# Kernel optimization log

Measured on AMD Instinct MI355X. Metric: run time of the kernel, lower is better.

## Reference

```python
import jax, jax.numpy as jnp
import numpy as np

B, T, D = 2, 2048, 1024
E, K, FF = 8, 2, 4096


def setup_inputs() -> dict:
    key = jax.random.key(0)
    ks = jax.random.split(key, 4)
    scale = 0.02
    return {
        "x": jax.random.normal(ks[0], (B, T, D), jnp.float32),
        "gate_w": jax.random.normal(ks[1], (D, E), jnp.float32) * scale,
        "gate_b": jnp.zeros((E,), jnp.float32),
        "w1": jax.random.normal(ks[2], (E, D, FF), jnp.float32) * scale,
        "b1": jnp.zeros((E, FF), jnp.float32),
        "w2": jax.random.normal(ks[3], (E, FF, D), jnp.float32) * scale,
        "b2": jnp.zeros((E, D), jnp.float32),
    }


def reference(x, gate_w, gate_b, w1, b1, w2, b2):
    # x: (B,T,D). Original runs every expert densely over all tokens then masks;
    # since mask*x == x at selected positions and output is re-masked, the math
    # equals: output[t] = sum_k softmax(topk_vals)[k] * expert_{idx_k}(x)[t].
    n_experts = w1.shape[0]
    gate_logits = x @ gate_w + gate_b                      # (B,T,E)
    topk_vals, topk_idx = jax.lax.top_k(gate_logits, K)    # (B,T,K)
    topk_w = jax.nn.softmax(topk_vals, axis=-1)            # (B,T,K)
    onehot = jax.nn.one_hot(topk_idx, n_experts, dtype=x.dtype)  # (B,T,K,E)
    comb = jnp.sum(onehot * topk_w[..., None], axis=2)     # (B,T,E) combine weights

    # Dense per-expert FFN over all tokens (faithful to original redundant compute)
    h = jax.nn.gelu(jnp.einsum('btd,edf->ebtf', x, w1) + b1[:, None, None, :],
                    approximate=False)                      # (E,B,T,FF)
    y = jnp.einsum('ebtf,efd->ebtd', h, w2) + b2[:, None, None, :]  # (E,B,T,D)
    output = jnp.einsum('ebtd,bte->btd', y, comb)           # (B,T,D)

    expert_counts = jnp.sum(onehot, axis=(0, 1, 2)).astype(jnp.float32)  # (E,)
    return output, gate_logits, topk_idx, expert_counts
```

## Files before the change

kernel.cpp:

```cpp
#include <hip/hip_runtime.h>
#include <math.h>

#define NTOK 4096
#define DIM  1024
#define NE   8
#define FF   4096

#define OUT_LOGITS 4194304
#define OUT_IDX    4227072
#define OUT_CNT    4235264

typedef unsigned short u16;
typedef __bf16 bf16x8 __attribute__((ext_vector_type(8)));
typedef float  f32x4  __attribute__((ext_vector_type(4)));
typedef u16    u16x8  __attribute__((ext_vector_type(8)));

__device__ __forceinline__ u16 f2bf(float f) {
  union { float f; unsigned u; } v; v.f = f;
  unsigned r = v.u + 0x7fffu + ((v.u >> 16) & 1u);
  return (u16)(r >> 16);
}

__device__ __forceinline__ float gelu_f(float v) {
  float u = v * (0.7978845608f + 0.0356774081f * v * v);
  float e = __expf(2.f * u);
  float t = 1.f - 2.f / (e + 1.f);
  return 0.5f * v * (1.f + t);
}

__device__ __forceinline__ void gload_lds16(const u16* g, u16* l) {
  __builtin_amdgcn_global_load_lds(
      (const __attribute__((address_space(1))) void*)(g),
      (__attribute__((address_space(3))) void*)(l), 16, 0, 0);
}

__global__ __launch_bounds__(256) void transpose_cvt2_kernel(
    const float* __restrict__ w1, u16* __restrict__ w1t,
    const float* __restrict__ w2, u16* __restrict__ w2t) {
  __shared__ float tile[4096];
  int id = blockIdx.x;
  const float* in; u16* out; int R, C, xt, yt, z;
  if (id < 8192) {
    in = w1; out = w1t; R = DIM; C = FF;
    xt = id & 63; yt = (id >> 6) & 15; z = id >> 10;
  } else {
    int i2 = id - 8192;
    in = w2; out = w2t; R = FF; C = DIM;
    xt = i2 & 15; yt = (i2 >> 4) & 63; z = i2 >> 10;
  }
  in  += (size_t)z * R * C;
  out += (size_t)z * R * C;
  const int c0 = xt * 64, r0 = yt * 64;
  const int t = threadIdx.x;

  {
    int cc = t & 15, rr = t >> 4;
    #pragma unroll
    for (int p = 0; p < 4; p++) {
      int r = rr + p * 16;
      float4 v = *(const float4*)(in + (size_t)(r0 + r) * C + c0 + cc * 4);
      *(float4*)&tile[r * 64 + ((cc ^ (r >> 3)) << 2)] = v;
    }
  }
  __syncthreads();
  {
    int h = t & 7, cg = t >> 3;
    #pragma unroll
    for (int p = 0; p < 2; p++) {
      int c = p * 32 + cg;
      int base = ((((c >> 2) ^ h) << 2)) + (c & 3);
      u16x8 o;
      #pragma unroll
      for (int j = 0; j < 8; j++)
        o[j] = f2bf(tile[(h * 8 + j) * 64 + base]);
      *(u16x8*)(out + (size_t)(c0 + c) * R + r0 + h * 8) = o;
    }
  }
}

__global__ __launch_bounds__(256) void gate_kernel(const float* __restrict__ x,
                                                   const float* __restrict__ gw,
                                                   const float* __restrict__ gb,
                                                   float* __restrict__ out,
                                                   int2* __restrict__ tk_idx,
                                                   float2* __restrict__ tk_w) {
  int wave = threadIdx.x >> 6, lane = threadIdx.x & 63;
  int token = blockIdx.x * 4 + wave;
  const float* xr = x + (size_t)token * DIM + lane * 16;
  float acc[NE];
  #pragma unroll
  for (int e = 0; e < NE; e++) acc[e] = 0.f;
  #pragma unroll
  for (int c = 0; c < 16; c += 4) {
    float4 xv = *(const float4*)(xr + c);
    const float* gwr = gw + (size_t)(lane * 16 + c) * NE;
    float xs[4] = {xv.x, xv.y, xv.z, xv.w};
    #pragma unroll
    for (int q = 0; q < 4; q++)
      #pragma unroll
      for (int e = 0; e < NE; e++)
        acc[e] += xs[q] * gwr[q * NE + e];
  }
  #pragma unroll
  for (int off = 32; off; off >>= 1)
    #pragma unroll
    for (int e = 0; e < NE; e++)
      acc[e] += __shfl_down(acc[e], off);

  if (lane == 0) {
    float lg[NE];
    #pragma unroll
    for (int e = 0; e < NE; e++) {
      lg[e] = acc[e] + gb[e];
      out[OUT_LOGITS + token * NE + e] = lg[e];
    }
    int i0 = 0; float v0 = lg[0];
    #pragma unroll
    for (int e = 1; e < NE; e++) if (lg[e] > v0) { v0 = lg[e]; i0 = e; }
    int i1 = -1; float v1 = -1e30f;
    #pragma unroll
    for (int e = 0; e < NE; e++) if (e != i0 && lg[e] > v1) { v1 = lg[e]; i1 = e; }
    float ex = expf(v1 - v0);
    float s = 1.f + ex;
    out[OUT_IDX + token * 2]     = (float)i0;
    out[OUT_IDX + token * 2 + 1] = (float)i1;
    tk_idx[token] = make_int2(i0, i1);
    tk_w[token]   = make_float2(1.f / s, ex / s);
  }
}

__global__ __launch_bounds__(512) void build_lists_kernel(
    const int2* __restrict__ tk_idx, const float2* __restrict__ tk_w,
    int* __restrict__ counts, int* __restrict__ offsets,
    int* __restrict__ tok_list, float* __restrict__ wt_list,
    float* __restrict__ cnt_out) {
  __shared__ int s_cnt[NE];
  int e = threadIdx.x >> 6, lane = threadIdx.x & 63;
  int cnt = 0;
  for (int base = 0; base < NTOK; base += 64) {
    int2 idx = tk_idx[base + lane];
    cnt += __popcll(__ballot(idx.x == e || idx.y == e));
  }
  if (lane == 0) s_cnt[e] = cnt;
  __syncthreads();
  int off = 0;
  for (int ee = 0; ee < e; ee++) off += s_cnt[ee];
  if (lane == 0) {
    counts[e]  = s_cnt[e];
    offsets[e] = off;
    cnt_out[e] = (float)s_cnt[e];
  }
  int pos = off;
  for (int base = 0; base < NTOK; base += 64) {
    int tok = base + lane;
    int2 idx = tk_idx[tok];
    float2 w = tk_w[tok];
    bool m0 = (idx.x == e), m1 = (idx.y == e);
    bool m = m0 || m1;
    unsigned long long mask = __ballot(m);
    if (m) {
      int p = pos + __popcll(mask & ((1ull << lane) - 1ull));
      tok_list[p] = tok;
      wt_list[p]  = m0 ? w.x : w.y;
    }
    pos += __popcll(mask);
  }
}

__global__ __launch_bounds__(256) void gather_x_kernel(const float* __restrict__ x,
                                                       const int* __restrict__ tok_list,
                                                       u16* __restrict__ xg) {
  int g = blockIdx.x;
  int tok = tok_list[g];
  int c = threadIdx.x * 4;
  float4 v = *(const float4*)(x + (size_t)tok * DIM + c);
  ushort4 o;
  o.x = f2bf(v.x); o.y = f2bf(v.y); o.z = f2bf(v.z); o.w = f2bf(v.w);
  *(ushort4*)(xg + (size_t)g * DIM + c) = o;
}

template <int MODE, int BM, int BN>
__global__ __launch_bounds__(512, 2) void moe_gemm2_kernel(
    const u16* __restrict__ Abase, const u16* __restrict__ Bbase,
    const float* __restrict__ bias,
    const int* __restrict__ counts, const int* __restrict__ offsets,
    const int* __restrict__ tok_list, const float* __restrict__ wt_list,
    u16* __restrict__ Hout, float* __restrict__ Out) {
  constexpr int KT = (MODE == 0) ? DIM : FF;
  constexpr int NT = (MODE == 0) ? FF : DIM;
  constexpr int LA = BM / 64;
  constexpr int LB = BN / 64;
  constexpr int MR = BM / 32;
  constexpr int NR = BN / 64;
  constexpr int ASZ = BM * 64;
  constexpr int BSZ = BN * 64;
  constexpr int NTILES = (MODE == 0) ? (KT / 64) : (KT / 128);

  extern __shared__ u16 sm[];

  const int zz = blockIdx.z;
  const int e  = (MODE == 1) ? (zz >> 1) : zz;
  const int koff = (MODE == 1) ? ((zz & 1) * (KT / 2)) : 0;
  const int ne = counts[e];
  const int m0 = blockIdx.y * BM;
  if (m0 >= ne) return;
  const int n0   = blockIdx.x * BN;
  const int offs = offsets[e];

  const int t = threadIdx.x;
  const int wave = t >> 6, lane = t & 63;
  const int quad = lane >> 4, l16 = lane & 15;
  const int wmb = (wave & 1) * (BM / 2);
  const int wnb = (wave >> 1) * (BN / 4);

  const u16* aptr[LA];
  const u16* bptr[LB];
  #pragma unroll
  for (int p = 0; p < LA; p++) {
    int idx = p * 512 + t;
    int row = idx >> 3, c = idx & 7;
    int clog = c ^ (row & 7);
    int s = m0 + row; if (s > ne - 1) s = ne - 1;
    aptr[p] = Abase + (size_t)(offs + s) * KT + koff + clog * 8;
  }
  #pragma unroll
  for (int p = 0; p < LB; p++) {
    int idx = p * 512 + t;
    int row = idx >> 3, c = idx & 7;
    int clog = c ^ (row & 7);
    bptr[p] = Bbase + ((size_t)e * NT + n0 + row) * KT + koff + clog * 8;
  }

  auto stage = [&](int buf, int k0) {
    #pragma unroll
    for (int p = 0; p < LA; p++)
      gload_lds16(aptr[p] + k0, sm + buf * ASZ + (p * 512 + t) * 8);
    #pragma unroll
    for (int p = 0; p < LB; p++)
      gload_lds16(bptr[p] + k0, sm + 2 * ASZ + buf * BSZ + (p * 512 + t) * 8);
  };

  const int xrow = l16 & 7;
  const int xo[2] = { ((0 + quad) ^ xrow) * 8, ((4 + quad) ^ xrow) * 8 };
  const int abase0 = (wmb + l16) * 64;
  const int bbase0 = 2 * ASZ + (wnb + l16) * 64;

  f32x4 acc[MR][NR];
  #pragma unroll
  for (int i = 0; i < MR; i++)
    #pragma unroll
    for (int j = 0; j < NR; j++)
      acc[i][j] = (f32x4){0.f, 0.f, 0.f, 0.f};

  stage(0, 0);
  __syncthreads();
  int cur = 0;
  for (int kt = 0; kt < NTILES; ++kt) {
    if (kt + 1 < NTILES) stage(cur ^ 1, (kt + 1) * 64);
    const u16* As = sm + cur * ASZ;
    const u16* Bs = sm + cur * BSZ;
    #pragma unroll
    for (int kk = 0; kk < 2; kk++) {
      bf16x8 a[MR], b[NR];
      #pragma unroll
      for (int i = 0; i < MR; i++) a[i] = *(const bf16x8*)&As[abase0 + i * 1024 + xo[kk]];
      #pragma unroll
      for (int j = 0; j < NR; j++) b[j] = *(const bf16x8*)&Bs[bbase0 + j * 1024 + xo[kk]];
      #pragma unroll
      for (int i = 0; i < MR; i++)
        #pragma unroll
        for (int j = 0; j < NR; j++)
          acc[i][j] = __builtin_amdgcn_mfma_f32_16x16x32_bf16(a[i], b[j], acc[i][j], 0, 0, 0);
    }
    __syncthreads();
    cur ^= 1;
  }

  if (MODE == 0) {
    const float* bb = bias + (size_t)e * FF + n0 + wnb;
    float bc[NR];
    #pragma unroll
    for (int j = 0; j < NR; j++) bc[j] = bb[j * 16 + l16];
    #pragma unroll
    for (int i = 0; i < MR; i++) {
      #pragma unroll
      for (int r = 0; r < 4; r++) {
        int s = m0 + wmb + i * 16 + quad * 4 + r;
        if (s < ne) {
          u16* hr = Hout + (size_t)(offs + s) * FF + n0 + wnb;
          #pragma unroll
          for (int j = 0; j < NR; j++)
            hr[j * 16 + l16] = f2bf(gelu_f(acc[i][j][r] + bc[j]));
        }
      }
    }
  } else {
    const float* bb = bias + (size_t)e * DIM + n0 + wnb;
    float bc[NR];
    #pragma unroll
    for (int j = 0; j < NR; j++) bc[j] = (zz & 1) ? 0.f : bb[j * 16 + l16];
    #pragma unroll
    for (int i = 0; i < MR; i++) {
      #pragma unroll
      for (int r = 0; r < 4; r++) {
        int s = m0 + wmb + i * 16 + quad * 4 + r;
        if (s < ne) {
          int   tok = tok_list[offs + s];
          float w   = wt_list[offs + s];
          float* orow = Out + (size_t)tok * DIM + n0 + wnb;
          #pragma unroll
          for (int j = 0; j < NR; j++)
            atomicAdd(&orow[j * 16 + l16], (acc[i][j][r] + bc[j]) * w);
        }
      }
    }
  }
}

extern "C" void kernel_launch(void* const* d_in, const int* in_sizes, int n_in,
                              void* d_out, int out_size, void* d_ws, size_t ws_size,
                              hipStream_t stream) {
  const float* x   = (const float*)d_in[0];
  const float* gw  = (const float*)d_in[1];
  const float* gb  = (const float*)d_in[2];
  const float* w1  = (const float*)d_in[3];
  const float* b1  = (const float*)d_in[4];
  const float* w2  = (const float*)d_in[5];
  const float* b2  = (const float*)d_in[6];
  float* out = (float*)d_out;
  char*  ws  = (char*)d_ws;

  u16* w1t = (u16*)(ws);
  u16* w2t = (u16*)(ws + 1ull * 67108864);
  u16* h   = (u16*)(ws + 2ull * 67108864);
  u16* xg  = (u16*)(ws + 3ull * 67108864);
  char* meta = ws + 3ull * 67108864 + 16777216;
  int*    counts   = (int*)(meta);
  int*    offsets  = (int*)(meta + 64);
  int*    tok_list = (int*)(meta + 128);
  float*  wt_list  = (float*)(meta + 128 + 32768);
  int2*   tk_idx   = (int2*)(meta + 128 + 2 * 32768);
  float2* tk_w     = (float2*)(meta + 128 + 2 * 32768 + 32768);
  (void)in_sizes; (void)n_in; (void)out_size; (void)ws_size;

  static bool attr_set = false;
  if (!attr_set) {
    hipFuncSetAttribute(reinterpret_cast<const void*>(moe_gemm2_kernel<0, 256, 256>),
                        hipFuncAttributeMaxDynamicSharedMemorySize, 131072);
    hipFuncSetAttribute(reinterpret_cast<const void*>(moe_gemm2_kernel<1, 128, 256>),
                        hipFuncAttributeMaxDynamicSharedMemorySize, 98304);
    attr_set = true;
  }

  hipMemsetAsync(out, 0, (size_t)OUT_LOGITS * 4, stream);

  transpose_cvt2_kernel<<<16384, 256, 0, stream>>>(w1, w1t, w2, w2t);
  gate_kernel<<<NTOK / 4, 256, 0, stream>>>(x, gw, gb, out, tk_idx, tk_w);
  build_lists_kernel<<<1, 512, 0, stream>>>(tk_idx, tk_w, counts, offsets, tok_list, wt_list,
                                            out + OUT_CNT);
  gather_x_kernel<<<2 * NTOK, 256, 0, stream>>>(x, tok_list, xg);

  moe_gemm2_kernel<0, 256, 256><<<dim3(FF / 256, NTOK / 256, NE), 512, 131072, stream>>>(
      xg, w1t, b1, counts, offsets, tok_list, wt_list, h, nullptr);
  moe_gemm2_kernel<1, 128, 256><<<dim3(DIM / 256, NTOK / 128, NE * 2), 512, 98304, stream>>>(
      h, w2t, b2, counts, offsets, tok_list, wt_list, nullptr, out);
}
```

Baseline: 636.3 us.

## Deepen MoE GEMM pipeline to four-stage ring with manual waitcnt and drop split-K

```diff
diff --git a/kernel.cpp b/kernel.cpp
--- a/kernel.cpp
+++ b/kernel.cpp
@@ -32,6 +32,17 @@
   __builtin_amdgcn_global_load_lds(
       (const __attribute__((address_space(1))) void*)(g),
       (__attribute__((address_space(3))) void*)(l), 16, 0, 0);
+}
+
+template <int N>
+__device__ __forceinline__ void wait_vm() {
+  if constexpr (N == 0)      asm volatile("s_waitcnt vmcnt(0)" ::: "memory");
+  else if constexpr (N == 1) asm volatile("s_waitcnt vmcnt(1)" ::: "memory");
+  else if constexpr (N == 2) asm volatile("s_waitcnt vmcnt(2)" ::: "memory");
+  else if constexpr (N == 3) asm volatile("s_waitcnt vmcnt(3)" ::: "memory");
+  else if constexpr (N == 4) asm volatile("s_waitcnt vmcnt(4)" ::: "memory");
+  else if constexpr (N == 6) asm volatile("s_waitcnt vmcnt(6)" ::: "memory");
+  else if constexpr (N == 8) asm volatile("s_waitcnt vmcnt(8)" ::: "memory");
 }
 
 __global__ __launch_bounds__(256) void transpose_cvt2_kernel(
@@ -180,7 +191,7 @@
 }
 
 template <int MODE, int BM, int BN>
-__global__ __launch_bounds__(512, 2) void moe_gemm2_kernel(
+__global__ __launch_bounds__(512, 2) void moe_gemm3_kernel(
     const u16* __restrict__ Abase, const u16* __restrict__ Bbase,
     const float* __restrict__ bias,
     const int* __restrict__ counts, const int* __restrict__ offsets,
@@ -188,19 +199,18 @@
     u16* __restrict__ Hout, float* __restrict__ Out) {
   constexpr int KT = (MODE == 0) ? DIM : FF;
   constexpr int NT = (MODE == 0) ? FF : DIM;
-  constexpr int LA = BM / 64;
-  constexpr int LB = BN / 64;
+  constexpr int NK = KT / 32;
+  constexpr int LA = BM / 128;
+  constexpr int LB = BN / 128;
+  constexpr int L  = LA + LB;
   constexpr int MR = BM / 32;
   constexpr int NR = BN / 64;
-  constexpr int ASZ = BM * 64;
-  constexpr int BSZ = BN * 64;
-  constexpr int NTILES = (MODE == 0) ? (KT / 64) : (KT / 128);
+  constexpr int ASLOT = BM * 32;
+  constexpr int BSLOT = BN * 32;
 
   extern __shared__ u16 sm[];
 
-  const int zz = blockIdx.z;
-  const int e  = (MODE == 1) ? (zz >> 1) : zz;
-  const int koff = (MODE == 1) ? ((zz & 1) * (KT / 2)) : 0;
+  const int e  = blockIdx.z;
   const int ne = counts[e];
   const int m0 = blockIdx.y * BM;
   if (m0 >= ne) return;
@@ -218,32 +228,31 @@
   #pragma unroll
   for (int p = 0; p < LA; p++) {
     int idx = p * 512 + t;
-    int row = idx >> 3, c = idx & 7;
-    int clog = c ^ (row & 7);
+    int row = idx >> 2, c = idx & 3;
+    int clog = c ^ ((row ^ (row >> 2)) & 3);
     int s = m0 + row; if (s > ne - 1) s = ne - 1;
-    aptr[p] = Abase + (size_t)(offs + s) * KT + koff + clog * 8;
+    aptr[p] = Abase + (size_t)(offs + s) * KT + clog * 8;
   }
   #pragma unroll
   for (int p = 0; p < LB; p++) {
     int idx = p * 512 + t;
-    int row = idx >> 3, c = idx & 7;
-    int clog = c ^ (row & 7);
-    bptr[p] = Bbase + ((size_t)e * NT + n0 + row) * KT + koff + clog * 8;
-  }
-
-  auto stage = [&](int buf, int k0) {
+    int row = idx >> 2, c = idx & 3;
+    int clog = c ^ ((row ^ (row >> 2)) & 3);
+    bptr[p] = Bbase + ((size_t)e * NT + n0 + row) * KT + clog * 8;
+  }
+
+  auto stage = [&](int slot, int kt) {
     #pragma unroll
     for (int p = 0; p < LA; p++)
-      gload_lds16(aptr[p] + k0, sm + buf * ASZ + (p * 512 + t) * 8);
+      gload_lds16(aptr[p] + kt * 32, sm + slot * ASLOT + (p * 512 + t) * 8);
     #pragma unroll
     for (int p = 0; p < LB; p++)
-      gload_lds16(bptr[p] + k0, sm + 2 * ASZ + buf * BSZ + (p * 512 + t) * 8);
+      gload_lds16(bptr[p] + kt * 32, sm + 4 * ASLOT + slot * BSLOT + (p * 512 + t) * 8);
   };
 
-  const int xrow = l16 & 7;
-  const int xo[2] = { ((0 + quad) ^ xrow) * 8, ((4 + quad) ^ xrow) * 8 };
-  const int abase0 = (wmb + l16) * 64;
-  const int bbase0 = 2 * ASZ + (wnb + l16) * 64;
+  const int csw = ((l16 ^ (l16 >> 2)) ^ quad) & 3;
+  const int aoff = (wmb + l16) * 32 + csw * 8;
+  const int boff = 4 * ASLOT + (wnb + l16) * 32 + csw * 8;
 
   f32x4 acc[MR][NR];
   #pragma unroll
@@ -252,29 +261,44 @@
     for (int j = 0; j < NR; j++)
       acc[i][j] = (f32x4){0.f, 0.f, 0.f, 0.f};
 
-  stage(0, 0);
-  __syncthreads();
-  int cur = 0;
-  for (int kt = 0; kt < NTILES; ++kt) {
-    if (kt + 1 < NTILES) stage(cur ^ 1, (kt + 1) * 64);
-    const u16* As = sm + cur * ASZ;
-    const u16* Bs = sm + cur * BSZ;
-    #pragma unroll
-    for (int kk = 0; kk < 2; kk++) {
-      bf16x8 a[MR], b[NR];
-      #pragma unroll
-      for (int i = 0; i < MR; i++) a[i] = *(const bf16x8*)&As[abase0 + i * 1024 + xo[kk]];
-      #pragma unroll
-      for (int j = 0; j < NR; j++) b[j] = *(const bf16x8*)&Bs[bbase0 + j * 1024 + xo[kk]];
-      #pragma unroll
-      for (int i = 0; i < MR; i++)
-        #pragma unroll
-        for (int j = 0; j < NR; j++)
-          acc[i][j] = __builtin_amdgcn_mfma_f32_16x16x32_bf16(a[i], b[j], acc[i][j], 0, 0, 0);
-    }
-    __syncthreads();
-    cur ^= 1;
-  }
+  auto compute = [&](int slot) {
+    const u16* As = sm + slot * ASLOT + aoff;
+    const u16* Bs = sm + slot * BSLOT + boff;
+    bf16x8 a[MR], b[NR];
+    #pragma unroll
+    for (int i = 0; i < MR; i++) a[i] = *(const bf16x8*)&As[i * 512];
+    #pragma unroll
+    for (int j = 0; j < NR; j++) b[j] = *(const bf16x8*)&Bs[j * 512];
+    __builtin_amdgcn_s_setprio(1);
+    #pragma unroll
+    for (int i = 0; i < MR; i++)
+      #pragma unroll
+      for (int j = 0; j < NR; j++)
+        acc[i][j] = __builtin_amdgcn_mfma_f32_16x16x32_bf16(a[i], b[j], acc[i][j], 0, 0, 0);
+    __builtin_amdgcn_s_setprio(0);
+  };
+
+  stage(0, 0); stage(1, 1); stage(2, 2);
+  wait_vm<2 * L>();
+  __builtin_amdgcn_s_barrier();
+  __builtin_amdgcn_sched_barrier(0);
+
+  for (int kt = 0; kt < NK - 3; ++kt) {
+    stage((kt + 3) & 3, kt + 3);
+    compute(kt & 3);
+    wait_vm<2 * L>();
+    __builtin_amdgcn_s_barrier();
+    __builtin_amdgcn_sched_barrier(0);
+  }
+  compute((NK - 3) & 3);
+  wait_vm<L>();
+  __builtin_amdgcn_s_barrier();
+  __builtin_amdgcn_sched_barrier(0);
+  compute((NK - 2) & 3);
+  wait_vm<0>();
+  __builtin_amdgcn_s_barrier();
+  __builtin_amdgcn_sched_barrier(0);
+  compute((NK - 1) & 3);
 
   if (MODE == 0) {
     const float* bb = bias + (size_t)e * FF + n0 + wnb;
@@ -298,7 +322,7 @@
     const float* bb = bias + (size_t)e * DIM + n0 + wnb;
     float bc[NR];
     #pragma unroll
-    for (int j = 0; j < NR; j++) bc[j] = (zz & 1) ? 0.f : bb[j * 16 + l16];
+    for (int j = 0; j < NR; j++) bc[j] = bb[j * 16 + l16];
     #pragma unroll
     for (int i = 0; i < MR; i++) {
       #pragma unroll
@@ -345,9 +369,9 @@
 
   static bool attr_set = false;
   if (!attr_set) {
-    hipFuncSetAttribute(reinterpret_cast<const void*>(moe_gemm2_kernel<0, 256, 256>),
+    hipFuncSetAttribute(reinterpret_cast<const void*>(moe_gemm3_kernel<0, 256, 256>),
                         hipFuncAttributeMaxDynamicSharedMemorySize, 131072);
-    hipFuncSetAttribute(reinterpret_cast<const void*>(moe_gemm2_kernel<1, 128, 256>),
+    hipFuncSetAttribute(reinterpret_cast<const void*>(moe_gemm3_kernel<1, 128, 256>),
                         hipFuncAttributeMaxDynamicSharedMemorySize, 98304);
     attr_set = true;
   }
@@ -360,8 +384,8 @@
                                             out + OUT_CNT);
   gather_x_kernel<<<2 * NTOK, 256, 0, stream>>>(x, tok_list, xg);
 
-  moe_gemm2_kernel<0, 256, 256><<<dim3(FF / 256, NTOK / 256, NE), 512, 131072, stream>>>(
+  moe_gemm3_kernel<0, 256, 256><<<dim3(FF / 256, NTOK / 256, NE), 512, 131072, stream>>>(
       xg, w1t, b1, counts, offsets, tok_list, wt_list, h, nullptr);
-  moe_gemm2_kernel<1, 128, 256><<<dim3(DIM / 256, NTOK / 128, NE * 2), 512, 98304, stream>>>(
+  moe_gemm3_kernel<1, 128, 256><<<dim3(DIM / 256, NTOK / 128, NE), 512, 98304, stream>>>(
       h, w2t, b2, counts, offsets, tok_list, wt_list, nullptr, out);
 }
```

After: 642.0 us. No clear change (+0.9%).
